# Optimization experiments

Hardware: AMD Instinct MI355X
Metric: run time of the kernel (lower is better)

The kernel has to match this reference:

```python
import jax, jax.numpy as jnp
import numpy as np

N_TAGS = 16
START_IX = 14
STOP_IX = 15
NEG = -10000.0

VOCAB = 100000
EMBED = 256
HID = 512          # bidirectional LSTM: per-direction hidden = HID // 2
H = HID // 2
T = 8192


def setup_inputs() -> dict:
    key = jax.random.key(0)
    ks = jax.random.split(key, 16)
    sentence = jax.random.randint(ks[0], (T,), 0, VOCAB)
    embed = jax.random.normal(ks[1], (VOCAB, EMBED), dtype=jnp.float32)
    # PyTorch LSTM params, gate order [i, f, g, o]
    s_ih = 1.0 / np.sqrt(H)
    w_ih_f = jax.random.uniform(ks[2], (4 * H, EMBED), minval=-s_ih, maxval=s_ih)
    w_hh_f = jax.random.uniform(ks[3], (4 * H, H), minval=-s_ih, maxval=s_ih)
    b_ih_f = jax.random.uniform(ks[4], (4 * H,), minval=-s_ih, maxval=s_ih)
    b_hh_f = jax.random.uniform(ks[5], (4 * H,), minval=-s_ih, maxval=s_ih)
    w_ih_b = jax.random.uniform(ks[6], (4 * H, EMBED), minval=-s_ih, maxval=s_ih)
    w_hh_b = jax.random.uniform(ks[7], (4 * H, H), minval=-s_ih, maxval=s_ih)
    b_ih_b = jax.random.uniform(ks[8], (4 * H,), minval=-s_ih, maxval=s_ih)
    b_hh_b = jax.random.uniform(ks[9], (4 * H,), minval=-s_ih, maxval=s_ih)
    # hid2tag linear
    s_o = 1.0 / np.sqrt(HID)
    W_out = jax.random.uniform(ks[10], (N_TAGS, HID), minval=-s_o, maxval=s_o)
    b_out = jax.random.uniform(ks[11], (N_TAGS,), minval=-s_o, maxval=s_o)
    # CRF transition: transition[i, j] = score of j -> i
    transition = jax.random.normal(ks[12], (N_TAGS, N_TAGS), dtype=jnp.float32)
    transition = transition.at[START_IX, :].set(NEG)
    transition = transition.at[:, STOP_IX].set(NEG)
    # random initial hidden state, as in _init_hidden (torch.randn)
    h0 = jax.random.normal(ks[13], (2, H), dtype=jnp.float32)
    c0 = jax.random.normal(ks[14], (2, H), dtype=jnp.float32)
    return {"sentence": sentence, "embed": embed,
            "w_ih_f": w_ih_f, "w_hh_f": w_hh_f, "b_ih_f": b_ih_f, "b_hh_f": b_hh_f,
            "w_ih_b": w_ih_b, "w_hh_b": w_hh_b, "b_ih_b": b_ih_b, "b_hh_b": b_hh_b,
            "W_out": W_out, "b_out": b_out, "transition": transition,
            "h0": h0, "c0": c0}


def _lstm_dir(xw, w_hh, h0, c0):
    # xw: [T, 4H] precomputed input projection (+ both biases)
    def step(carry, xw_t):
        h, c = carry
        z = xw_t + h @ w_hh.T
        i, f, g, o = jnp.split(z, 4)
        i = jax.nn.sigmoid(i)
        f = jax.nn.sigmoid(f)
        g = jnp.tanh(g)
        o = jax.nn.sigmoid(o)
        c = f * c + i * g
        h = o * jnp.tanh(c)
        return (h, c), h
    _, hs = jax.lax.scan(step, (h0, c0), xw)
    return hs  # [T, H]


def _feats(sentence, embed, w_ih_f, w_hh_f, b_ih_f, b_hh_f,
           w_ih_b, w_hh_b, b_ih_b, b_hh_b, W_out, b_out, h0, c0):
    emb = embed[sentence]                                   # [T, E]
    xw_f = emb @ w_ih_f.T + (b_ih_f + b_hh_f)               # [T, 4H]
    hs_f = _lstm_dir(xw_f, w_hh_f, h0[0], c0[0])            # [T, H]
    xw_b = emb[::-1] @ w_ih_b.T + (b_ih_b + b_hh_b)
    hs_b = _lstm_dir(xw_b, w_hh_b, h0[1], c0[1])[::-1]      # [T, H]
    hs = jnp.concatenate([hs_f, hs_b], axis=-1)             # [T, 2H]
    return hs @ W_out.T + b_out                             # [T, n_tags]


def reference(sentence, embed, w_ih_f, w_hh_f, b_ih_f, b_hh_f,
              w_ih_b, w_hh_b, b_ih_b, b_hh_b, W_out, b_out,
              transition, h0, c0):
    feats = _feats(sentence, embed, w_ih_f, w_hh_f, b_ih_f, b_hh_f,
                   w_ih_b, w_hh_b, b_ih_b, b_hh_b, W_out, b_out, h0, c0)

    fv0 = jnp.full((N_TAGS,), NEG, dtype=feats.dtype).at[START_IX].set(0.0)

    def viterbi_step(fv, feat):
        # temp[i, j] = fv[j] + feat[i] + transition[i, j]
        temp = fv[None, :] + feat[:, None] + transition
        return temp.max(axis=1), jnp.argmax(temp, axis=1)

    fv, bps = jax.lax.scan(viterbi_step, fv0, feats)        # bps: [T, n_tags]
    fv = fv + transition[:, STOP_IX]
    id_last = jnp.argmax(fv)

    def backtrack(idc, bp_t):
        return bp_t[idc], idc

    _, path = jax.lax.scan(backtrack, id_last, bps, reverse=True)
    return path  # [T] best tag per timestep
```

## Files before the change

kernel.cpp:

```cpp
#include <hip/hip_runtime.h>
#include <cstdint>
#include <cstddef>

#define T_LEN 8192
#define EMB 256
#define HD 256
#define G4 1024
#define NT 16
#define START_IX 14
#define STOP_IX 15

#define SLICE 8
#define ROWSD 32
#define WPAD 260
#define SENT 0xFFFFFFFFu
#define NSCAN 32

#define MB(d, p, s, j) ((((size_t)(d) * 2 + (p)) * 32 + (s)) * 8 + (j))

struct ScanS {
    float wf[ROWSD * WPAD];
    float wb[ROWSD * WPAD];
    float hf[256];
    float hb[256];
    float part[ROWSD * 17];
    float xwf[2][ROWSD];
    float xwb[2][ROWSD];
};
struct GemmS {
    float at[32][65];
    float bt[128][65];
};
#define SMEM_BYTES 83968

__device__ __forceinline__ unsigned poll_dual(
    const unsigned long long* __restrict__ fsrc,
    const unsigned* __restrict__ ssrc, unsigned t)
{
#pragma unroll 1
    for (int it = 0; it < (1 << 20); ++it) {
        unsigned long long u;
        asm volatile("global_load_dwordx2 %0, %1, off sc0\n\t"
                     "s_waitcnt vmcnt(0)"
                     : "=v"(u) : "v"(fsrc) : "memory");
        if ((unsigned)(u >> 32) == t) return (unsigned)u;
        unsigned v = __hip_atomic_load(ssrc, __ATOMIC_RELAXED,
                                       __HIP_MEMORY_SCOPE_AGENT);
        if (v != SENT) return v;
    }
    return 0u;
}

__device__ __forceinline__ unsigned poll_sent(const unsigned* p) {
    unsigned v; int spin = 0;
    do {
        v = __hip_atomic_load(p, __ATOMIC_RELAXED, __HIP_MEMORY_SCOPE_AGENT);
    } while (v == SENT && ++spin < (1 << 20));
    return v;
}

__global__ __launch_bounds__(512) void k_fused(
    const int* __restrict__ sent, const float* __restrict__ embed,
    const float* __restrict__ wih_f, const float* __restrict__ wih_b,
    const float* __restrict__ bih_f, const float* __restrict__ bhh_f,
    const float* __restrict__ bih_b, const float* __restrict__ bhh_b,
    const float* __restrict__ whh_f, const float* __restrict__ whh_b,
    const float* __restrict__ h0, const float* __restrict__ c0,
    float* __restrict__ xw, float* __restrict__ h_hist,
    unsigned long long* __restrict__ mbox)
{
    __shared__ __align__(16) char smraw[SMEM_BYTES];
    const int tid = threadIdx.x;

    if ((blockIdx.x & 7) != 0) {
        GemmS* G = (GemmS*)smraw;
        const int f = (blockIdx.x >> 3) * 7 + (blockIdx.x & 7) - 1;
        const int tx = tid & 31, ty = tid >> 5;
        for (int u = f; u < 4096; u += 224) {
            const int t_tile = u >> 4, sub = u & 15;
            const int dir = sub >> 3, r_tile = sub & 7;
            const float* __restrict__ wih = dir ? wih_b : wih_f;
            const float* __restrict__ bih = dir ? bih_b : bih_f;
            const float* __restrict__ bhh = dir ? bhh_b : bhh_f;
            const int t0 = t_tile * 32, r0 = r_tile * 128;
            float acc[2][4] = {};
            for (int k0 = 0; k0 < EMB; k0 += 64) {
                __syncthreads();
                for (int i = tid; i < 32 * 64; i += 512) {
                    int row = i >> 6, k = i & 63;
                    int t = t0 + row;
                    int ts = dir ? (T_LEN - 1 - t) : t;
                    G->at[row][k] = embed[(size_t)sent[ts] * EMB + k0 + k];
                }
                for (int i = tid; i < 128 * 64; i += 512) {
                    int row = i >> 6, k = i & 63;
                    G->bt[row][k] = wih[(size_t)(r0 + row) * EMB + k0 + k];
                }
                __syncthreads();
#pragma unroll 16
                for (int kc = 0; kc < 64; ++kc) {
                    float a[2], b[4];
#pragma unroll
                    for (int v = 0; v < 2; ++v) a[v] = G->at[ty * 2 + v][kc];
#pragma unroll
                    for (int v = 0; v < 4; ++v) b[v] = G->bt[tx * 4 + v][kc];
#pragma unroll
                    for (int v = 0; v < 2; ++v)
#pragma unroll
                        for (int w = 0; w < 4; ++w) acc[v][w] += a[v] * b[w];
                }
            }
#pragma unroll
            for (int v = 0; v < 2; ++v) {
                int t = t0 + ty * 2 + v;
#pragma unroll
                for (int w = 0; w < 4; ++w) {
                    int r = r0 + tx * 4 + w;
                    float val = acc[v][w] + bih[r] + bhh[r];
                    __hip_atomic_store(
                        (unsigned*)&xw[((size_t)dir * T_LEN + t) * G4 + r],
                        __float_as_uint(val),
                        __ATOMIC_RELAXED, __HIP_MEMORY_SCOPE_AGENT);
                }
            }
        }
        return;
    }

    ScanS* S = (ScanS*)smraw;
    const int wsl = blockIdx.x >> 3;
    const int wave = tid >> 6, lane = tid & 63;

    for (int i = tid; i < ROWSD * 256; i += 512) {
        int r = i >> 8, k = i & 255;
        int R = ((r >> 3) << 8) + wsl * SLICE + (r & 7);
        S->wf[r * WPAD + k] = whh_f[(size_t)R * HD + k];
        S->wb[r * WPAD + k] = whh_b[(size_t)R * HD + k];
    }
    if (tid < 256) { S->hf[tid] = h0[tid]; S->hb[tid] = h0[256 + tid]; }
    float c_f = 0.f, c_b = 0.f;
    if (wave == 0 && lane < 8) {
        c_f = c0[wsl * SLICE + lane];
        c_b = c0[256 + wsl * SLICE + lane];
    }
    if (tid < 64) {
        int d = tid >> 5, row = tid & 31;
        int R = ((row >> 3) << 8) + wsl * SLICE + (row & 7);
        unsigned v = poll_sent(
            (const unsigned*)&xw[((size_t)d * T_LEN) * G4 + R]);
        (d ? S->xwb : S->xwf)[0][row] = __uint_as_float(v);
    }
    __syncthreads();

    float* __restrict__ hhf = h_hist;
    float* __restrict__ hhb = h_hist + (size_t)T_LEN * HD;

    for (int t = 0; t < T_LEN; ++t) {
        const int cur = t & 1, nxt = cur ^ 1;

        {
            const int q = tid >> 5, rr = tid & 31;
            const float4* wr = (const float4*)&S->wf[rr * WPAD + q * 16];
            const float4* hp = (const float4*)&S->hf[q * 16];
            float a0 = 0.f, a1 = 0.f, a2 = 0.f, a3 = 0.f;
#pragma unroll
            for (int i = 0; i < 4; ++i) {
                float4 wv = wr[i], hv = hp[i];
                a0 += wv.x * hv.x; a1 += wv.y * hv.y;
                a2 += wv.z * hv.z; a3 += wv.w * hv.w;
            }
            S->part[rr * 17 + q] = (a0 + a1) + (a2 + a3);
        }
        __syncthreads();

        if (wave == 0) {
            const int r = lane & 31;
            float z = S->xwf[cur][r];
#pragma unroll
            for (int q = 0; q < 16; ++q) z += S->part[r * 17 + q];
            float a = ((r >> 3) == 2) ? tanhf(z) : 1.f / (1.f + expf(-z));
            const int j = lane & 7;
            float af = __shfl(a, 8 + j);
            float ag = __shfl(a, 16 + j);
            float ao = __shfl(a, 24 + j);
            if (lane < 8) {
                c_f = af * c_f + a * ag;
                float hv = ao * tanhf(c_f);
                S->hf[wsl * SLICE + j] = hv;
                unsigned long long pkt =
                    ((unsigned long long)(unsigned)t << 32)
                    | (unsigned long long)__float_as_uint(hv);
                mbox[MB(0, cur, wsl, j)] = pkt;
                __hip_atomic_store(
                    (unsigned*)&hhf[(size_t)t * HD + wsl * SLICE + j],
                    __float_as_uint(hv),
                    __ATOMIC_RELAXED, __HIP_MEMORY_SCOPE_AGENT);
            }
        } else if (wave <= 4) {
            if (t > 0) {
                const int idx = (wave - 1) * 64 + lane;
                unsigned v = poll_dual(
                    &mbox[MB(1, (t - 1) & 1, idx >> 3, idx & 7)],
                    (const unsigned*)&hhb[(size_t)(t - 1) * HD + idx],
                    (unsigned)(t - 1));
                S->hb[idx] = __uint_as_float(v);
            }
        } else if (wave == 5) {
            if (t + 1 < T_LEN) {
                int d = lane >> 5, row = lane & 31;
                int R = ((row >> 3) << 8) + wsl * SLICE + (row & 7);
                unsigned v = poll_sent((const unsigned*)
                    &xw[((size_t)d * T_LEN + t + 1) * G4 + R]);
                (d ? S->xwb : S->xwf)[nxt][row] = __uint_as_float(v);
            }
        }
        __syncthreads();

        {
            const int q = tid >> 5, rr = tid & 31;
            const float4* wr = (const float4*)&S->wb[rr * WPAD + q * 16];
            const float4* hp = (const float4*)&S->hb[q * 16];
            float a0 = 0.f, a1 = 0.f, a2 = 0.f, a3 = 0.f;
#pragma unroll
            for (int i = 0; i < 4; ++i) {
                float4 wv = wr[i], hv = hp[i];
                a0 += wv.x * hv.x; a1 += wv.y * hv.y;
                a2 += wv.z * hv.z; a3 += wv.w * hv.w;
            }
            S->part[rr * 17 + q] = (a0 + a1) + (a2 + a3);
        }
        __syncthreads();

        if (wave == 0) {
            const int r = lane & 31;
            float z = S->xwb[cur][r];
#pragma unroll
            for (int q = 0; q < 16; ++q) z += S->part[r * 17 + q];
            float a = ((r >> 3) == 2) ? tanhf(z) : 1.f / (1.f + expf(-z));
            const int j = lane & 7;
            float af = __shfl(a, 8 + j);
            float ag = __shfl(a, 16 + j);
            float ao = __shfl(a, 24 + j);
            if (lane < 8) {
                c_b = af * c_b + a * ag;
                float hv = ao * tanhf(c_b);
                S->hb[wsl * SLICE + j] = hv;
                unsigned long long pkt =
                    ((unsigned long long)(unsigned)t << 32)
                    | (unsigned long long)__float_as_uint(hv);
                mbox[MB(1, cur, wsl, j)] = pkt;
                __hip_atomic_store(
                    (unsigned*)&hhb[(size_t)t * HD + wsl * SLICE + j],
                    __float_as_uint(hv),
                    __ATOMIC_RELAXED, __HIP_MEMORY_SCOPE_AGENT);
            }
        } else if (wave <= 4) {
            const int idx = (wave - 1) * 64 + lane;
            unsigned v = poll_dual(
                &mbox[MB(0, cur, idx >> 3, idx & 7)],
                (const unsigned*)&hhf[(size_t)t * HD + idx], (unsigned)t);
            S->hf[idx] = __uint_as_float(v);
        }
        __syncthreads();
    }
}

__global__ __launch_bounds__(256) void k_feats(
    const float* __restrict__ h_hist, const float* __restrict__ Wout,
    const float* __restrict__ bout, float* __restrict__ feats)
{
    __shared__ float wlds[16][512];
    const int tid = threadIdx.x;
    for (int i = tid; i < 16 * 512; i += 256) wlds[i >> 9][i & 511] = Wout[i];
    __syncthreads();
    const int idx = blockIdx.x * 256 + tid;
    const int t = idx >> 2, tg = (idx & 3) * 4;
    const float4* hf = (const float4*)(h_hist + (size_t)t * HD);
    const float4* hb = (const float4*)(h_hist + (size_t)(T_LEN + (T_LEN - 1 - t)) * HD);
    float acc[4];
#pragma unroll
    for (int g = 0; g < 4; ++g) acc[g] = bout[tg + g];
    for (int k = 0; k < 64; ++k) {
        float4 a = hf[k];
#pragma unroll
        for (int g = 0; g < 4; ++g) {
            float4 b = *(const float4*)&wlds[tg + g][k * 4];
            acc[g] += a.x * b.x + a.y * b.y + a.z * b.z + a.w * b.w;
        }
    }
    for (int k = 0; k < 64; ++k) {
        float4 a = hb[k];
#pragma unroll
        for (int g = 0; g < 4; ++g) {
            float4 b = *(const float4*)&wlds[tg + g][256 + k * 4];
            acc[g] += a.x * b.x + a.y * b.y + a.z * b.z + a.w * b.w;
        }
    }
#pragma unroll
    for (int g = 0; g < 4; ++g) feats[(size_t)t * NT + tg + g] = acc[g];
}

__device__ __forceinline__ unsigned bsel16(uint4 g, unsigned e) {
    unsigned wd = (e < 8u) ? ((e < 4u) ? g.x : g.y) : ((e < 12u) ? g.z : g.w);
    return (wd >> ((e & 3u) * 8u)) & 15u;
}

__global__ __launch_bounds__(256) void k_viterbi(
    const float* __restrict__ feats, const float* __restrict__ trans,
    int* __restrict__ out, unsigned char* __restrict__ bp)
{
    __shared__ int sid;
    __shared__ unsigned slo[512], shi[512];
    const int tid = threadIdx.x;

    if (tid < 64) {
        const int i = tid & 15, jg = tid >> 4;
        double tr[4];
#pragma unroll
        for (int u = 0; u < 4; ++u) tr[u] = (double)trans[i * 16 + jg * 4 + u];
        double fvn = (i == START_IX) ? 0.0 : -10000.0;
        float fA = feats[i];
        float fB = feats[16 + i];

        for (int t = 0; t < T_LEN; ++t) {
            float fC = (t + 2 < T_LEN) ? feats[(size_t)(t + 2) * NT + i] : 0.f;

            double best = -1e300; int bj = 0;
#pragma unroll
            for (int u = 0; u < 4; ++u) {
                double fvv = __shfl(fvn, jg * 4 + u);
                double v = fvv + tr[u];
                if (v > best) { best = v; bj = jg * 4 + u; }
            }
            double ob = __shfl_down(best, 32); int oj = __shfl_down(bj, 32);
            if (ob > best || (ob == best && oj < bj)) { best = ob; bj = oj; }
            ob = __shfl_down(best, 16); oj = __shfl_down(bj, 16);
            if (ob > best || (ob == best && oj < bj)) { best = ob; bj = oj; }

            if (tid < 16) {
                bp[(size_t)t * 16 + i] = (unsigned char)bj;
                fvn = (double)fA + best;
            }
            fA = fB; fB = fC;
        }
        double term = (tid < 16) ? fvn + (double)trans[tid * 16 + STOP_IX] : -1e300;
        int ti = tid;
#pragma unroll
        for (int off = 1; off < 16; off <<= 1) {
            double ov = __shfl_xor(term, off); int oi = __shfl_xor(ti, off);
            if (ov > term || (ov == term && oi < ti)) { term = ov; ti = oi; }
        }
        if (tid == 0) sid = ti;
    }
    __syncthreads();

    const int j = tid;
    unsigned Flo = 0x76543210u, Fhi = 0xfedcba98u;
    for (int t = 32 * j + 31; t >= 32 * j; --t) {
        uint4 g = *(const uint4*)&bp[(size_t)t * 16];
        unsigned nlo = 0, nhi = 0;
#pragma unroll
        for (int x = 0; x < 8; ++x) {
            unsigned e = (Flo >> (x * 4)) & 15u;
            nlo |= bsel16(g, e) << (x * 4);
        }
#pragma unroll
        for (int x = 0; x < 8; ++x) {
            unsigned e = (Fhi >> (x * 4)) & 15u;
            nhi |= bsel16(g, e) << (x * 4);
        }
        Flo = nlo; Fhi = nhi;
    }
    slo[j] = Flo; shi[j] = Fhi;
    slo[j + 256] = 0x76543210u; shi[j + 256] = 0xfedcba98u;
    __syncthreads();
    for (int off = 1; off < 256; off <<= 1) {
        unsigned alo = slo[j], ahi = shi[j];
        unsigned blo = slo[j + off], bhi = shi[j + off];
        __syncthreads();
        unsigned nlo = 0, nhi = 0;
#pragma unroll
        for (int x = 0; x < 8; ++x) {
            unsigned e = (blo >> (x * 4)) & 15u;
            unsigned rr = ((e < 8u ? alo : ahi) >> ((e & 7u) * 4u)) & 15u;
            nlo |= rr << (x * 4);
        }
#pragma unroll
        for (int x = 0; x < 8; ++x) {
            unsigned e = (bhi >> (x * 4)) & 15u;
            unsigned rr = ((e < 8u ? alo : ahi) >> ((e & 7u) * 4u)) & 15u;
            nhi |= rr << (x * 4);
        }
        slo[j] = nlo; shi[j] = nhi;
        __syncthreads();
    }
    int idl = sid;
    unsigned plo = slo[j + 1], phi = shi[j + 1];
    unsigned x = (((unsigned)idl < 8u ? plo : phi) >> (((unsigned)idl & 7u) * 4u)) & 15u;
    out[32 * j + 31] = (int)x;
    for (int t = 32 * j + 30; t >= 32 * j; --t) {
        x = (unsigned)bp[(size_t)(t + 1) * 16 + x];
        out[t] = (int)x;
    }
}

extern "C" void kernel_launch(void* const* d_in, const int* in_sizes, int n_in,
                              void* d_out, int out_size, void* d_ws, size_t ws_size,
                              hipStream_t stream) {
    const int*   sent  = (const int*)  d_in[0];
    const float* embed = (const float*)d_in[1];
    const float* wih_f = (const float*)d_in[2];
    const float* whh_f = (const float*)d_in[3];
    const float* bih_f = (const float*)d_in[4];
    const float* bhh_f = (const float*)d_in[5];
    const float* wih_b = (const float*)d_in[6];
    const float* whh_b = (const float*)d_in[7];
    const float* bih_b = (const float*)d_in[8];
    const float* bhh_b = (const float*)d_in[9];
    const float* Wout  = (const float*)d_in[10];
    const float* bout  = (const float*)d_in[11];
    const float* trans = (const float*)d_in[12];
    const float* h0    = (const float*)d_in[13];
    const float* c0    = (const float*)d_in[14];
    int* out = (int*)d_out;

    float* ws_xw   = (float*)d_ws;
    float* ws_h    = ws_xw + (size_t)2 * T_LEN * G4;
    float* ws_feat = ws_h + (size_t)2 * T_LEN * HD;
    unsigned char* ws_bp = (unsigned char*)(ws_feat + (size_t)T_LEN * NT);
    unsigned long long* ws_mbox =
        (unsigned long long*)(ws_bp + (size_t)T_LEN * NT);

    hipMemsetAsync(ws_xw, 0xFF, (size_t)2 * T_LEN * G4 * sizeof(float), stream);
    hipMemsetAsync(ws_h, 0xFF, (size_t)2 * T_LEN * HD * sizeof(float), stream);
    hipMemsetAsync(ws_mbox, 0xFF, 1024 * sizeof(unsigned long long), stream);

    k_fused<<<256, 512, 0, stream>>>(sent, embed, wih_f, wih_b,
                                     bih_f, bhh_f, bih_b, bhh_b,
                                     whh_f, whh_b, h0, c0,
                                     ws_xw, ws_h, ws_mbox);
    k_feats<<<128, 256, 0, stream>>>(ws_h, Wout, bout, ws_feat);
    k_viterbi<<<1, 256, 0, stream>>>(ws_feat, trans, out, ws_bp);
}
```

Baseline: 14.97 ms.

## Merge forward and backward LSTM recurrence phases into one step per timestep

The scan loop previously ran the forward and backward directions as two sequential phases per timestep, each with its own matvec, gate update and cross-block mailbox poll, separated by four block barriers. Now both directions' weight slices share one LDS array: each wave computes partial dot products for all 64 rows, wave 0 and wave 1 apply the gates for forward and backward in parallel, and waves 2-7 poll the other blocks' forward and backward hidden values plus the next xw rows. This halves the barriers and the serialized inter-block exchange rounds per step. In exchange, each thread does longer dot products, and one set of pollers must wait on both directions, skipping its own slice.

Result: slower. 24.56 ms (+64.0%).

```diff
diff --git a/kernel.cpp b/kernel.cpp
--- a/kernel.cpp
+++ b/kernel.cpp
@@ -11,21 +11,19 @@
 #define STOP_IX 15
 
 #define SLICE 8
-#define ROWSD 32
+#define ROWS2 64
 #define WPAD 260
 #define SENT 0xFFFFFFFFu
-#define NSCAN 32
 
 #define MB(d, p, s, j) ((((size_t)(d) * 2 + (p)) * 32 + (s)) * 8 + (j))
 
 struct ScanS {
-    float wf[ROWSD * WPAD];
-    float wb[ROWSD * WPAD];
+    float w[ROWS2 * WPAD];
     float hf[256];
     float hb[256];
-    float part[ROWSD * 17];
-    float xwf[2][ROWSD];
-    float xwb[2][ROWSD];
+    float part[ROWS2 * 9];
+    float xwf[2][32];
+    float xwb[2][32];
 };
 struct GemmS {
     float at[32][65];
@@ -131,18 +129,16 @@
     const int wsl = blockIdx.x >> 3;
     const int wave = tid >> 6, lane = tid & 63;
 
-    for (int i = tid; i < ROWSD * 256; i += 512) {
+    for (int i = tid; i < ROWS2 * 256; i += 512) {
         int r = i >> 8, k = i & 255;
-        int R = ((r >> 3) << 8) + wsl * SLICE + (r & 7);
-        S->wf[r * WPAD + k] = whh_f[(size_t)R * HD + k];
-        S->wb[r * WPAD + k] = whh_b[(size_t)R * HD + k];
+        int dir = r >> 5, lr = r & 31;
+        int R = ((lr >> 3) << 8) + wsl * SLICE + (lr & 7);
+        S->w[r * WPAD + k] = (dir ? whh_b : whh_f)[(size_t)R * HD + k];
     }
     if (tid < 256) { S->hf[tid] = h0[tid]; S->hb[tid] = h0[256 + tid]; }
     float c_f = 0.f, c_b = 0.f;
-    if (wave == 0 && lane < 8) {
-        c_f = c0[wsl * SLICE + lane];
-        c_b = c0[256 + wsl * SLICE + lane];
-    }
+    if (wave == 0 && lane < 8) c_f = c0[wsl * SLICE + lane];
+    if (wave == 1 && lane < 8) c_b = c0[256 + wsl * SLICE + lane];
     if (tid < 64) {
         int d = tid >> 5, row = tid & 31;
         int R = ((row >> 3) << 8) + wsl * SLICE + (row & 7);
@@ -159,17 +155,17 @@
         const int cur = t & 1, nxt = cur ^ 1;
 
         {
-            const int q = tid >> 5, rr = tid & 31;
-            const float4* wr = (const float4*)&S->wf[rr * WPAD + q * 16];
-            const float4* hp = (const float4*)&S->hf[q * 16];
+            const float4* wr = (const float4*)&S->w[lane * WPAD + wave * 32];
+            const float4* hp = (const float4*)
+                ((lane < 32 ? S->hf : S->hb) + wave * 32);
             float a0 = 0.f, a1 = 0.f, a2 = 0.f, a3 = 0.f;
 #pragma unroll
-            for (int i = 0; i < 4; ++i) {
+            for (int i = 0; i < 8; ++i) {
                 float4 wv = wr[i], hv = hp[i];
                 a0 += wv.x * hv.x; a1 += wv.y * hv.y;
                 a2 += wv.z * hv.z; a3 += wv.w * hv.w;
             }
-            S->part[rr * 17 + q] = (a0 + a1) + (a2 + a3);
+            S->part[lane * 9 + wave] = (a0 + a1) + (a2 + a3);
         }
         __syncthreads();
 
@@ -177,9 +173,9 @@
             const int r = lane & 31;
             float z = S->xwf[cur][r];
 #pragma unroll
-            for (int q = 0; q < 16; ++q) z += S->part[r * 17 + q];
+            for (int s = 0; s < 8; ++s) z += S->part[r * 9 + s];
             float a = ((r >> 3) == 2) ? tanhf(z) : 1.f / (1.f + expf(-z));
-            const int j = lane & 7;
+            const int j = r & 7;
             float af = __shfl(a, 8 + j);
             float ag = __shfl(a, 16 + j);
             float ao = __shfl(a, 24 + j);
@@ -196,48 +192,13 @@
                     __float_as_uint(hv),
                     __ATOMIC_RELAXED, __HIP_MEMORY_SCOPE_AGENT);
             }
-        } else if (wave <= 4) {
-            if (t > 0) {
-                const int idx = (wave - 1) * 64 + lane;
-                unsigned v = poll_dual(
-                    &mbox[MB(1, (t - 1) & 1, idx >> 3, idx & 7)],
-                    (const unsigned*)&hhb[(size_t)(t - 1) * HD + idx],
-                    (unsigned)(t - 1));
-                S->hb[idx] = __uint_as_float(v);
-            }
-        } else if (wave == 5) {
-            if (t + 1 < T_LEN) {
-                int d = lane >> 5, row = lane & 31;
-                int R = ((row >> 3) << 8) + wsl * SLICE + (row & 7);
-                unsigned v = poll_sent((const unsigned*)
-                    &xw[((size_t)d * T_LEN + t + 1) * G4 + R]);
-                (d ? S->xwb : S->xwf)[nxt][row] = __uint_as_float(v);
-            }
-        }
-        __syncthreads();
-
-        {
-            const int q = tid >> 5, rr = tid & 31;
-            const float4* wr = (const float4*)&S->wb[rr * WPAD + q * 16];
-            const float4* hp = (const float4*)&S->hb[q * 16];
-            float a0 = 0.f, a1 = 0.f, a2 = 0.f, a3 = 0.f;
-#pragma unroll
-            for (int i = 0; i < 4; ++i) {
-                float4 wv = wr[i], hv = hp[i];
-                a0 += wv.x * hv.x; a1 += wv.y * hv.y;
-                a2 += wv.z * hv.z; a3 += wv.w * hv.w;
-            }
-            S->part[rr * 17 + q] = (a0 + a1) + (a2 + a3);
-        }
-        __syncthreads();
-
-        if (wave == 0) {
+        } else if (wave == 1) {
             const int r = lane & 31;
             float z = S->xwb[cur][r];
 #pragma unroll
-            for (int q = 0; q < 16; ++q) z += S->part[r * 17 + q];
+            for (int s = 0; s < 8; ++s) z += S->part[(32 + r) * 9 + s];
             float a = ((r >> 3) == 2) ? tanhf(z) : 1.f / (1.f + expf(-z));
-            const int j = lane & 7;
+            const int j = r & 7;
             float af = __shfl(a, 8 + j);
             float ag = __shfl(a, 16 + j);
             float ao = __shfl(a, 24 + j);
@@ -254,12 +215,34 @@
                     __float_as_uint(hv),
                     __ATOMIC_RELAXED, __HIP_MEMORY_SCOPE_AGENT);
             }
-        } else if (wave <= 4) {
-            const int idx = (wave - 1) * 64 + lane;
-            unsigned v = poll_dual(
-                &mbox[MB(0, cur, idx >> 3, idx & 7)],
-                (const unsigned*)&hhf[(size_t)t * HD + idx], (unsigned)t);
-            S->hf[idx] = __uint_as_float(v);
+        } else {
+            const int p = (wave - 2) * 64 + lane;
+#pragma unroll 1
+            for (int item = p; item < 576; item += 384) {
+                if (item < 256) {
+                    int s = item >> 3;
+                    if (s == wsl) continue;
+                    unsigned v = poll_dual(
+                        &mbox[MB(0, cur, s, item & 7)],
+                        (const unsigned*)&hhf[(size_t)t * HD + item],
+                        (unsigned)t);
+                    S->hf[item] = __uint_as_float(v);
+                } else if (item < 512) {
+                    int e = item - 256, s = e >> 3;
+                    if (s == wsl) continue;
+                    unsigned v = poll_dual(
+                        &mbox[MB(1, cur, s, e & 7)],
+                        (const unsigned*)&hhb[(size_t)t * HD + e],
+                        (unsigned)t);
+                    S->hb[e] = __uint_as_float(v);
+                } else if (t + 1 < T_LEN) {
+                    int e = item - 512, d = e >> 5, row = e & 31;
+                    int R = ((row >> 3) << 8) + wsl * SLICE + (row & 7);
+                    unsigned v = poll_sent((const unsigned*)
+                        &xw[((size_t)d * T_LEN + t + 1) * G4 + R]);
+                    (d ? S->xwb : S->xwf)[nxt][row] = __uint_as_float(v);
+                }
+            }
         }
         __syncthreads();
     }
```
